# Kernel tuning notes

Measured on AMD Instinct MI355X. Metric: run time of the kernel, lower is better.

The kernel has to match this reference:

```python
import jax, jax.numpy as jnp
import numpy as np

H = 8  # number of heads


def setup_inputs() -> dict:
    key = jax.random.key(0)
    ks = jax.random.split(key, 5)
    B, L, D = 4, 2048, 512
    scale = 1.0 / np.sqrt(D)
    return {
        "query": jax.random.normal(ks[0], (B, L, D), dtype=jnp.float32),
        "keys": jax.random.normal(ks[1], (B, L, D), dtype=jnp.float32),
        "Wq": jax.random.normal(ks[2], (D, D), dtype=jnp.float32) * scale,
        "Wk": jax.random.normal(ks[3], (D, D), dtype=jnp.float32) * scale,
        "Wv": jax.random.normal(ks[4], (D, D), dtype=jnp.float32) * scale,
    }


def reference(query, keys, Wq, Wk, Wv):
    B, Lq, D = query.shape
    Lk = keys.shape[1]
    dh = D // H
    # Linear layers (torch nn.Linear: y = x @ W.T), then split heads.
    Q = (query @ Wq.T).reshape(B, Lq, H, dh)
    K = (keys @ Wk.T).reshape(B, Lk, H, dh)
    V = (keys @ Wv.T).reshape(B, Lk, H, dh)
    # NOTE: original scales by sqrt(key_dim) == sqrt(D), not sqrt(head_dim).
    inv_scale = 1.0 / jnp.sqrt(jnp.float32(D))
    scores = jnp.einsum("bqhd,bkhd->bhqk", Q, K) * inv_scale  # [B,H,Lq,Lk]
    attn = jax.nn.softmax(scores, axis=-1)
    # dropout_p = 0 (eval); no dropout applied.
    out = jnp.einsum("bhqk,bkhd->bqhd", attn, V).reshape(B, Lq, D)
    return out + query  # residual
```

## Files before the change

### kernel.cpp

```cpp
#include <hip/hip_runtime.h>

typedef unsigned short u16;
typedef unsigned int   u32;
typedef short  s16x8  __attribute__((ext_vector_type(8)));
typedef float  f32x16 __attribute__((ext_vector_type(16)));
typedef unsigned int u32x2 __attribute__((ext_vector_type(2)));

__device__ __forceinline__ u16 f2bf(float f) {
    union { u32 i; float f; } x; x.f = f;
    return (u16)((x.i + 0x8000u) >> 16);
}
__device__ __forceinline__ u32 cvt_pk_bf16(float a, float b) {
    u32 r;
    asm("v_cvt_pk_bf16_f32 %0, %1, %2" : "=v"(r) : "v"(a), "v"(b));
    return r;
}
__device__ __forceinline__ u32x2 pl32_swap2(u32 vdst, u32 vsrc) {
#if __has_builtin(__builtin_amdgcn_permlane32_swap)
    return __builtin_amdgcn_permlane32_swap(vdst, vsrc, false, false);
#else
    asm("v_permlane32_swap_b32 %0, %1" : "+v"(vdst), "+v"(vsrc));
    u32x2 r; r.x = vdst; r.y = vsrc; return r;
#endif
}

#define PD 512

__global__ __launch_bounds__(256) void proj_mfma(
    const float* __restrict__ query, const float* __restrict__ keys,
    const float* __restrict__ Wq, const float* __restrict__ Wk, const float* __restrict__ Wv,
    u16* __restrict__ Qo, u16* __restrict__ Ko, u16* __restrict__ Vt)
{
    const int z = blockIdx.z;
    const float* __restrict__ X = (z == 0) ? query : keys;
    const float* __restrict__ W = (z == 0) ? Wq : ((z == 1) ? Wk : Wv);
    const int bx = blockIdx.x;
    const int by = blockIdx.y;

    const float* __restrict__ Amat = (z < 2) ? X : W;
    const float* __restrict__ Bmat = (z < 2) ? W : X;
    const int a0 = ((z < 2) ? bx : by) * 128;
    const int b0 = ((z < 2) ? by : bx) * 128;

    __shared__ u16 As[128][40];
    __shared__ u16 Bs[128][40];

    const int tid  = threadIdx.x;
    const int wave = tid >> 6, lane = tid & 63;
    const int wm = wave >> 1, wn = wave & 1;
    const int l31 = lane & 31, lh = lane >> 5;

    const int srow = tid >> 1;
    const int sk   = (tid & 1) * 16;

    f32x16 acc[2][2];
    #pragma unroll
    for (int i = 0; i < 2; ++i)
        #pragma unroll
        for (int j = 0; j < 2; ++j)
            #pragma unroll
            for (int r = 0; r < 16; ++r) acc[i][j][r] = 0.f;

    float4 ra[4], rb[4];
    {
        const float* ap = Amat + (size_t)(a0 + srow) * PD + sk;
        const float* bp = Bmat + (size_t)(b0 + srow) * PD + sk;
        #pragma unroll
        for (int i = 0; i < 4; ++i) {
            ra[i] = *(const float4*)(ap + 4*i);
            rb[i] = *(const float4*)(bp + 4*i);
        }
    }

    for (int k0 = 0; k0 < PD; k0 += 32) {
        __syncthreads();
        {
            u32 aw[8], bw[8];
            #pragma unroll
            for (int i = 0; i < 4; ++i) {
                aw[2*i]   = cvt_pk_bf16(ra[i].x, ra[i].y);
                aw[2*i+1] = cvt_pk_bf16(ra[i].z, ra[i].w);
                bw[2*i]   = cvt_pk_bf16(rb[i].x, rb[i].y);
                bw[2*i+1] = cvt_pk_bf16(rb[i].z, rb[i].w);
            }
            *(uint4*)&As[srow][sk]     = *(uint4*)&aw[0];
            *(uint4*)&As[srow][sk + 8] = *(uint4*)&aw[4];
            *(uint4*)&Bs[srow][sk]     = *(uint4*)&bw[0];
            *(uint4*)&Bs[srow][sk + 8] = *(uint4*)&bw[4];
        }
        if (k0 + 32 < PD) {
            const float* ap = Amat + (size_t)(a0 + srow) * PD + (k0 + 32) + sk;
            const float* bp = Bmat + (size_t)(b0 + srow) * PD + (k0 + 32) + sk;
            #pragma unroll
            for (int i = 0; i < 4; ++i) {
                ra[i] = *(const float4*)(ap + 4*i);
                rb[i] = *(const float4*)(bp + 4*i);
            }
        }
        __syncthreads();

        #pragma unroll
        for (int ks = 0; ks < 2; ++ks) {
            s16x8 af[2], bfr[2];
            #pragma unroll
            for (int mf = 0; mf < 2; ++mf) {
                uint4 v = *(uint4*)&As[wm*64 + mf*32 + l31][ks*16 + lh*8];
                af[mf] = *(s16x8*)&v;
            }
            #pragma unroll
            for (int nf = 0; nf < 2; ++nf) {
                uint4 v = *(uint4*)&Bs[wn*64 + nf*32 + l31][ks*16 + lh*8];
                bfr[nf] = *(s16x8*)&v;
            }
            #pragma unroll
            for (int mf = 0; mf < 2; ++mf)
                #pragma unroll
                for (int nf = 0; nf < 2; ++nf)
                    acc[mf][nf] = __builtin_amdgcn_mfma_f32_32x32x16_bf16(
                        af[mf], bfr[nf], acc[mf][nf], 0, 0, 0);
        }
    }

    const float osc = (z == 0) ? (0.044194173824159216f * 1.4426950408889634f) : 1.0f;
    u16* __restrict__ O = (z == 0) ? Qo : Ko;
    #pragma unroll
    for (int mf = 0; mf < 2; ++mf)
        #pragma unroll
        for (int nf = 0; nf < 2; ++nf)
            #pragma unroll
            for (int r = 0; r < 16; ++r) {
                const int mi = a0 + wm*64 + mf*32 + (r & 3) + 8*(r >> 2) + 4*lh;
                const int ni = b0 + wn*64 + nf*32 + l31;
                const u16 v = f2bf(acc[mf][nf][r] * osc);
                if (z < 2) {
                    O[(size_t)mi * PD + ni] = v;
                } else {
                    const int bb_ = ni >> 11, ll = ni & 2047;
                    Vt[((size_t)(bb_ * 512 + mi)) * 2048 + ll] = v;
                }
            }
}

__global__ __launch_bounds__(512) void attn_mfma(
    const u16* __restrict__ Qp, const u16* __restrict__ Kp, const u16* __restrict__ Vt,
    const float* __restrict__ query, float* __restrict__ out)
{
    const int flat = blockIdx.x + 16 * blockIdx.y + 128 * blockIdx.z;
    const int src  = (flat & 7) * 64 + (flat >> 3);
    const int qt = src & 15;
    const int h  = (src >> 4) & 7;
    const int b  = src >> 7;
    const int q0 = qt * 128;
    const int L = 2048;

    __shared__ uint4 lds_u4[73728 / 16];
    u16* lds16 = (u16*)lds_u4;

    const int tid  = threadIdx.x;
    const int wave = tid >> 6;
    const int grp  = wave >> 2;
    const int sw   = wave & 3;
    const int lane = tid & 63;
    const int l31 = lane & 31, lh = lane >> 5;

    u16* gb16 = lds16 + grp * 18432;
    u16* Ks   = gb16;
    u16* Vts  = gb16 + 4608;
    u16* Ks2  = gb16 + 9216;
    u16* Vts2 = gb16 + 13824;

    const int qrow = b * L + q0 + sw * 32 + l31;
    s16x8 qf[4];
    #pragma unroll
    for (int ds = 0; ds < 4; ++ds) {
        uint4 v = *(const uint4*)(Qp + (size_t)qrow * PD + h*64 + ds*16 + lh*8);
        qf[ds] = *(s16x8*)&v;
    }

    f32x16 ot[2];
    #pragma unroll
    for (int mf = 0; mf < 2; ++mf)
        #pragma unroll
        for (int r = 0; r < 16; ++r) ot[mf][r] = 0.f;
    float l_i = 0.f;

    const int gtid = tid & 255;
    const int srow = gtid >> 2;
    const int sc   = (gtid & 3) * 16;

    const u16* kpB = Kp + (size_t)(b*L + grp*128 + srow) * PD + h*64 + sc;
    const u16* vpB = Vt + ((size_t)((b*8 + h)*64 + srow)) * 2048 + grp*128 + sc;

    uint4 rk0, rk1, rv0, rv1;
    uint4 rk2, rk3, rv2, rv3;

#define A_LOADG(k0v) { \
    const u16* kp_ = kpB + (size_t)(k0v) * PD; \
    const u16* vp_ = vpB + (k0v); \
    rk0 = *(const uint4*)kp_;              rk1 = *(const uint4*)(kp_ + 8); \
    rv0 = *(const uint4*)vp_;              rv1 = *(const uint4*)(vp_ + 8); \
    rk2 = *(const uint4*)(kp_ + 64*PD);    rk3 = *(const uint4*)(kp_ + 64*PD + 8); \
    rv2 = *(const uint4*)(vp_ + 64);       rv3 = *(const uint4*)(vp_ + 64 + 8); }

#define A_STOREL() { \
    *(uint4*)&Ks  [srow*72 + sc]      = rk0; \
    *(uint4*)&Ks  [srow*72 + sc + 8]  = rk1; \
    *(uint4*)&Vts [srow*72 + sc]      = rv0; \
    *(uint4*)&Vts [srow*72 + sc + 8]  = rv1; \
    *(uint4*)&Ks2 [srow*72 + sc]      = rk2; \
    *(uint4*)&Ks2 [srow*72 + sc + 8]  = rk3; \
    *(uint4*)&Vts2[srow*72 + sc]      = rv2; \
    *(uint4*)&Vts2[srow*72 + sc + 8]  = rv3; }

    auto compute = [&](const u16* Ksb, const u16* Vtsb) {
        f32x16 s[2];
        #pragma unroll
        for (int kf = 0; kf < 2; ++kf) {
            #pragma unroll
            for (int r = 0; r < 16; ++r) s[kf][r] = 0.f;
            #pragma unroll
            for (int ds = 0; ds < 4; ++ds) {
                uint4 av = *(uint4*)&Ksb[(kf*32 + l31)*72 + ds*16 + lh*8];
                s[kf] = __builtin_amdgcn_mfma_f32_32x32x16_bf16(
                    *(s16x8*)&av, qf[ds], s[kf], 0, 0, 0);
            }
        }
        float rs = 0.f;
        u32 pq[2][4][2];
        #pragma unroll
        for (int kf = 0; kf < 2; ++kf)
            #pragma unroll
            for (int g = 0; g < 4; ++g) {
                float p0 = __builtin_amdgcn_exp2f(s[kf][4*g+0]);
                float p1 = __builtin_amdgcn_exp2f(s[kf][4*g+1]);
                float p2 = __builtin_amdgcn_exp2f(s[kf][4*g+2]);
                float p3 = __builtin_amdgcn_exp2f(s[kf][4*g+3]);
                rs += (p0 + p1) + (p2 + p3);
                pq[kf][g][0] = cvt_pk_bf16(p0, p1);
                pq[kf][g][1] = cvt_pk_bf16(p2, p3);
            }
        rs += __shfl_xor(rs, 32);
        l_i += rs;
        #pragma unroll
        for (int s4 = 0; s4 < 4; ++s4) {
            const int kf = s4 >> 1, ga = (s4 & 1) * 2;
            u32x2 r0 = pl32_swap2(pq[kf][ga][0], pq[kf][ga+1][0]);
            u32x2 r1 = pl32_swap2(pq[kf][ga][1], pq[kf][ga+1][1]);
            union { u32 w[4]; s16x8 v; } bu;
            bu.w[0] = r0.x; bu.w[1] = r1.x; bu.w[2] = r0.y; bu.w[3] = r1.y;
            #pragma unroll
            for (int mf = 0; mf < 2; ++mf) {
                uint4 av = *(uint4*)&Vtsb[(mf*32 + l31)*72 + s4*16 + lh*8];
                ot[mf] = __builtin_amdgcn_mfma_f32_32x32x16_bf16(
                    *(s16x8*)&av, bu.v, ot[mf], 0, 0, 0);
            }
        }
    };

    A_LOADG(0);
    #pragma unroll 1
    for (int j = 0; j < 8; ++j) {
        __syncthreads();
        A_STOREL();
        if (j + 1 < 8) A_LOADG((j + 1) * 256);
        __syncthreads();
        __builtin_amdgcn_s_setprio(1);
        compute(Ks,  Vts);
        compute(Ks2, Vts2);
        __builtin_amdgcn_s_setprio(0);
    }

    float* Ppart = (float*)lds_u4;
    float* l_p   = Ppart + 128*68;
    float* Oe    = (float*)lds_u4;

    __syncthreads();
    if (grp == 1) {
        #pragma unroll
        for (int mf = 0; mf < 2; ++mf)
            #pragma unroll
            for (int g = 0; g < 4; ++g) {
                float4 v;
                v.x = ot[mf][g*4+0]; v.y = ot[mf][g*4+1];
                v.z = ot[mf][g*4+2]; v.w = ot[mf][g*4+3];
                const int dh0 = mf*32 + 8*g + 4*lh;
                *(float4*)&Ppart[(sw*32 + l31)*68 + dh0] = v;
            }
        if (lh == 0) l_p[sw*32 + l31] = l_i;
    }
    __syncthreads();
    if (grp == 0) {
        const float inv_l = 1.0f / (l_i + l_p[sw*32 + l31]);
        #pragma unroll
        for (int mf = 0; mf < 2; ++mf)
            #pragma unroll
            for (int g = 0; g < 4; ++g) {
                const int dh0 = mf*32 + 8*g + 4*lh;
                float4 pv = *(float4*)&Ppart[(sw*32 + l31)*68 + dh0];
                ot[mf][g*4+0] = (ot[mf][g*4+0] + pv.x) * inv_l;
                ot[mf][g*4+1] = (ot[mf][g*4+1] + pv.y) * inv_l;
                ot[mf][g*4+2] = (ot[mf][g*4+2] + pv.z) * inv_l;
                ot[mf][g*4+3] = (ot[mf][g*4+3] + pv.w) * inv_l;
            }
    }
    __syncthreads();
    if (grp == 0) {
        #pragma unroll
        for (int mf = 0; mf < 2; ++mf)
            #pragma unroll
            for (int g = 0; g < 4; ++g) {
                float4 v;
                v.x = ot[mf][g*4+0]; v.y = ot[mf][g*4+1];
                v.z = ot[mf][g*4+2]; v.w = ot[mf][g*4+3];
                const int dh0 = mf*32 + 8*g + 4*lh;
                *(float4*)&Oe[(sw*32 + l31)*68 + dh0] = v;
            }
    }
    __syncthreads();
    {
        const int r  = tid >> 2;
        const int c0 = (tid & 3) * 16;
        const size_t gb = ((size_t)(b*L + q0 + r)) * PD + h*64 + c0;
        #pragma unroll
        for (int i = 0; i < 4; ++i) {
            float4 ov = *(float4*)&Oe[r*68 + c0 + 4*i];
            float4 qv = *(const float4*)(query + gb + 4*i);
            ov.x += qv.x; ov.y += qv.y; ov.z += qv.z; ov.w += qv.w;
            *(float4*)(out + gb + 4*i) = ov;
        }
    }
}

extern "C" void kernel_launch(void* const* d_in, const int* in_sizes, int n_in,
                              void* d_out, int out_size, void* d_ws, size_t ws_size,
                              hipStream_t stream) {
    const float* query = (const float*)d_in[0];
    const float* keys  = (const float*)d_in[1];
    const float* Wq    = (const float*)d_in[2];
    const float* Wk    = (const float*)d_in[3];
    const float* Wv    = (const float*)d_in[4];
    float* out = (float*)d_out;

    u16* Qp = (u16*)d_ws;
    u16* Kp = Qp + (size_t)8192 * 512;
    u16* Vt = Kp + (size_t)8192 * 512;

    proj_mfma<<<dim3(64, 4, 3), 256, 0, stream>>>(query, keys, Wq, Wk, Wv, Qp, Kp, Vt);
    attn_mfma<<<dim3(16, 8, 4), 512, 0, stream>>>(Qp, Kp, Vt, query, out);
}
```

Baseline: 159.2 us.

## Deepen projection K-tile to 64, remap block order, raise MFMA priority

```diff
diff --git a/kernel.cpp b/kernel.cpp
--- a/kernel.cpp
+++ b/kernel.cpp
@@ -26,24 +26,27 @@
 
 #define PD 512
 
-__global__ __launch_bounds__(256) void proj_mfma(
+__global__ __launch_bounds__(256, 3) void proj_mfma(
     const float* __restrict__ query, const float* __restrict__ keys,
     const float* __restrict__ Wq, const float* __restrict__ Wk, const float* __restrict__ Wv,
     u16* __restrict__ Qo, u16* __restrict__ Ko, u16* __restrict__ Vt)
 {
-    const int z = blockIdx.z;
+    const int flat = blockIdx.x + 64 * blockIdx.y + 256 * blockIdx.z;
+    const int src  = (flat & 7) * 96 + (flat >> 3);
+    const int by = src & 3;
+    const int bx = (src >> 2) & 63;
+    const int z  = src >> 8;
+
     const float* __restrict__ X = (z == 0) ? query : keys;
     const float* __restrict__ W = (z == 0) ? Wq : ((z == 1) ? Wk : Wv);
-    const int bx = blockIdx.x;
-    const int by = blockIdx.y;
 
     const float* __restrict__ Amat = (z < 2) ? X : W;
     const float* __restrict__ Bmat = (z < 2) ? W : X;
     const int a0 = ((z < 2) ? bx : by) * 128;
     const int b0 = ((z < 2) ? by : bx) * 128;
 
-    __shared__ u16 As[128][40];
-    __shared__ u16 Bs[128][40];
+    __shared__ u16 As[128][72];
+    __shared__ u16 Bs[128][72];
 
     const int tid  = threadIdx.x;
     const int wave = tid >> 6, lane = tid & 63;
@@ -51,7 +54,7 @@
     const int l31 = lane & 31, lh = lane >> 5;
 
     const int srow = tid >> 1;
-    const int sk   = (tid & 1) * 16;
+    const int sk2  = (tid & 1) * 32;
 
     f32x16 acc[2][2];
     #pragma unroll
@@ -61,46 +64,47 @@
             #pragma unroll
             for (int r = 0; r < 16; ++r) acc[i][j][r] = 0.f;
 
-    float4 ra[4], rb[4];
-    {
-        const float* ap = Amat + (size_t)(a0 + srow) * PD + sk;
-        const float* bp = Bmat + (size_t)(b0 + srow) * PD + sk;
-        #pragma unroll
-        for (int i = 0; i < 4; ++i) {
-            ra[i] = *(const float4*)(ap + 4*i);
-            rb[i] = *(const float4*)(bp + 4*i);
-        }
-    }
-
-    for (int k0 = 0; k0 < PD; k0 += 32) {
+    const float* apB = Amat + (size_t)(a0 + srow) * PD + sk2;
+    const float* bpB = Bmat + (size_t)(b0 + srow) * PD + sk2;
+
+    float4 ra[8], rb[8];
+    #pragma unroll
+    for (int i = 0; i < 8; ++i) {
+        ra[i] = *(const float4*)(apB + 4*i);
+        rb[i] = *(const float4*)(bpB + 4*i);
+    }
+
+    for (int k0 = 0; k0 < PD; k0 += 64) {
         __syncthreads();
         {
-            u32 aw[8], bw[8];
-            #pragma unroll
-            for (int i = 0; i < 4; ++i) {
+            u32 aw[16], bw[16];
+            #pragma unroll
+            for (int i = 0; i < 8; ++i) {
                 aw[2*i]   = cvt_pk_bf16(ra[i].x, ra[i].y);
                 aw[2*i+1] = cvt_pk_bf16(ra[i].z, ra[i].w);
                 bw[2*i]   = cvt_pk_bf16(rb[i].x, rb[i].y);
                 bw[2*i+1] = cvt_pk_bf16(rb[i].z, rb[i].w);
             }
-            *(uint4*)&As[srow][sk]     = *(uint4*)&aw[0];
-            *(uint4*)&As[srow][sk + 8] = *(uint4*)&aw[4];
-            *(uint4*)&Bs[srow][sk]     = *(uint4*)&bw[0];
-            *(uint4*)&Bs[srow][sk + 8] = *(uint4*)&bw[4];
-        }
-        if (k0 + 32 < PD) {
-            const float* ap = Amat + (size_t)(a0 + srow) * PD + (k0 + 32) + sk;
-            const float* bp = Bmat + (size_t)(b0 + srow) * PD + (k0 + 32) + sk;
-            #pragma unroll
-            for (int i = 0; i < 4; ++i) {
+            #pragma unroll
+            for (int q = 0; q < 4; ++q) {
+                *(uint4*)&As[srow][sk2 + 8*q] = *(uint4*)&aw[4*q];
+                *(uint4*)&Bs[srow][sk2 + 8*q] = *(uint4*)&bw[4*q];
+            }
+        }
+        if (k0 + 64 < PD) {
+            const float* ap = apB + (k0 + 64);
+            const float* bp = bpB + (k0 + 64);
+            #pragma unroll
+            for (int i = 0; i < 8; ++i) {
                 ra[i] = *(const float4*)(ap + 4*i);
                 rb[i] = *(const float4*)(bp + 4*i);
             }
         }
         __syncthreads();
 
-        #pragma unroll
-        for (int ks = 0; ks < 2; ++ks) {
+        __builtin_amdgcn_s_setprio(1);
+        #pragma unroll
+        for (int ks = 0; ks < 4; ++ks) {
             s16x8 af[2], bfr[2];
             #pragma unroll
             for (int mf = 0; mf < 2; ++mf) {
@@ -119,6 +123,7 @@
                     acc[mf][nf] = __builtin_amdgcn_mfma_f32_32x32x16_bf16(
                         af[mf], bfr[nf], acc[mf][nf], 0, 0, 0);
         }
+        __builtin_amdgcn_s_setprio(0);
     }
 
     const float osc = (z == 0) ? (0.044194173824159216f * 1.4426950408889634f) : 1.0f;
```

Result: slower. 185.1 us (+16.2%).
